# Kernel tuning notes

Measured on AMD Instinct MI355X. Metric: run time of the kernel, lower is better.

The kernel has to match this reference:

```python
import jax, jax.numpy as jnp
import numpy as np

B, S, C = 4, 4096, 128
C4 = C // 4  # q/k channels
OUT = 128    # == in_features, required by value @ weight


def setup_inputs() -> dict:
    key = jax.random.key(0)
    ks = jax.random.split(key, 9)
    stdv = 1.0 / np.sqrt(OUT)
    u = lambda k, shape, s: jax.random.uniform(k, shape, jnp.float32, -s, s)
    kaiming = lambda k, shape: u(k, shape, float(1.0 / np.sqrt(shape[1])))
    return {
        "x": jax.random.normal(ks[0], (B, S, C), jnp.float32),
        "weight": u(ks[1], (C, OUT), stdv),      # GCN weight [in, out]
        "bias": u(ks[2], (OUT,), stdv),
        "wq": kaiming(ks[3], (C4, C)),           # conv1d k=1 == linear [out_ch, in_ch]
        "bq": u(ks[4], (C4,), float(1.0 / np.sqrt(C))),
        "wk": kaiming(ks[5], (C4, C)),
        "bk": u(ks[6], (C4,), float(1.0 / np.sqrt(C))),
        "wv": kaiming(ks[7], (OUT, C)),
        "bv": u(ks[8], (OUT,), float(1.0 / np.sqrt(C))),
    }


def reference(x, weight, bias, wq, bq, wk, bk, wv, bv):
    # conv1d with kernel_size=1 == per-position linear projection
    q = jnp.einsum("bsc,qc->bsq", x, wq) + bq        # [B,S,C4] (query, pre-permute it is [B,C4,S])
    k = jnp.einsum("bsc,qc->bsq", x, wk) + bk        # [B,S,C4]
    # scores[i,j] = key_i . query_j  (unscaled), softmax over j
    scores = jnp.einsum("bic,bjc->bij", k, q)        # [B,S,S]
    adj = jax.nn.softmax(scores, axis=-1)
    v = jnp.einsum("bsc,oc->bso", x, wv) + bv        # [B,S,OUT]
    support = jnp.einsum("bso,ou->bsu", v, weight)   # [B,S,OUT]
    out = jnp.einsum("bij,bju->biu", adj, support)   # [B,S,OUT]
    return out + bias
```

## Files before the change

kernel.cpp:

```cpp
#include <hip/hip_runtime.h>

#define NB   4
#define SEQ  4096
#define CIN  128
#define C4D  32
#define OUTC 128
#define LOG2E 1.44269504f

typedef __attribute__((ext_vector_type(8))) short bf16x8;
typedef __attribute__((ext_vector_type(4))) float f32x4;

__device__ __forceinline__ short f2bf(float f) {
  union { float f; unsigned u; } v; v.f = f;
  unsigned r = v.u + 0x7FFFu + ((v.u >> 16) & 1u);
  return (short)(r >> 16);
}

__device__ __forceinline__ unsigned cvt_pk_bf16(float lo, float hi) {
  unsigned r;
  asm("v_cvt_pk_bf16_f32 %0, %1, %2" : "=v"(r) : "v"(lo), "v"(hi));
  return r;
}

__device__ __forceinline__ float fast_exp2(float x) {
  float r;
  asm("v_exp_f32 %0, %1" : "=v"(r) : "v"(x));
  return r;
}

__device__ __forceinline__ f32x4 mfma16(bf16x8 a, bf16x8 b, f32x4 c) {
  return __builtin_amdgcn_mfma_f32_16x16x32_bf16(a, b, c, 0, 0, 0);
}

__device__ __forceinline__ void gload_lds16(const short* g, short* l) {
  __builtin_amdgcn_global_load_lds(
      (const __attribute__((address_space(1))) void*)(g),
      (__attribute__((address_space(3))) void*)(l), 16, 0, 0);
}

__global__ void k_fuse(const float* __restrict__ wq, const float* __restrict__ wk,
                       const float* __restrict__ wv, const float* __restrict__ weight,
                       const float* __restrict__ bv,
                       short* __restrict__ wqb, short* __restrict__ wkb,
                       short* __restrict__ wfT, float* __restrict__ bfu) {
  int u = blockIdx.x, c = threadIdx.x;
  float acc = 0.f;
  for (int o = 0; o < OUTC; ++o) acc += wv[o * CIN + c] * weight[o * OUTC + u];
  wfT[u * CIN + c] = f2bf(acc);
  if (u < C4D) {
    wqb[u * CIN + c] = f2bf(wq[u * CIN + c]);
    wkb[u * CIN + c] = f2bf(wk[u * CIN + c]);
  }
  if (c == 0) {
    float a = 0.f;
    for (int o = 0; o < OUTC; ++o) a += bv[o] * weight[o * OUTC + u];
    bfu[u] = a;
  }
}

__global__ __launch_bounds__(256) void k_proj(
    const float* __restrict__ x, const float* __restrict__ bq, const float* __restrict__ bk,
    const short* __restrict__ wqb, const short* __restrict__ wkb,
    const short* __restrict__ wfT, const float* __restrict__ bfu,
    short* __restrict__ ql, short* __restrict__ kb, short* __restrict__ vfb) {
  const int wid = threadIdx.x >> 6, lane = threadIdx.x & 63;
  const int lo = lane & 15, g = lane >> 4;
  const int p0 = blockIdx.x * 64 + wid * 16;

  f32x4 aq[2] = {}, ak[2] = {}, as_[8] = {};

#pragma unroll
  for (int kk = 0; kk < 4; ++kk) {
    const float* xp = x + (size_t)(p0 + lo) * CIN + kk * 32 + g * 8;
    float4 xa = *(const float4*)xp;
    float4 xb = *(const float4*)(xp + 4);
    bf16x8 af;
    af[0] = f2bf(xa.x); af[1] = f2bf(xa.y); af[2] = f2bf(xa.z); af[3] = f2bf(xa.w);
    af[4] = f2bf(xb.x); af[5] = f2bf(xb.y); af[6] = f2bf(xb.z); af[7] = f2bf(xb.w);
#pragma unroll
    for (int n = 0; n < 2; ++n) {
      bf16x8 bq_ = *(const bf16x8*)(wqb + (size_t)(n * 16 + lo) * CIN + kk * 32 + g * 8);
      aq[n] = mfma16(af, bq_, aq[n]);
      bf16x8 bk_ = *(const bf16x8*)(wkb + (size_t)(n * 16 + lo) * CIN + kk * 32 + g * 8);
      ak[n] = mfma16(af, bk_, ak[n]);
    }
#pragma unroll
    for (int n = 0; n < 8; ++n) {
      bf16x8 bs = *(const bf16x8*)(wfT + (size_t)(n * 16 + lo) * CIN + kk * 32 + g * 8);
      as_[n] = mfma16(af, bs, as_[n]);
    }
  }

#pragma unroll
  for (int n = 0; n < 2; ++n) {
    float bqv = bq[n * 16 + lo], bkv = bk[n * 16 + lo];
    int u = n * 16 + lo;
#pragma unroll
    for (int r = 0; r < 4; ++r) {
      int p = p0 + 4 * g + r;
      int bb = p >> 12, s = p & (SEQ - 1);
      ql[(size_t)bb * (SEQ * 32) + (size_t)(s >> 5) * 1024 + ((s >> 4) & 1) * 512 +
         (u >> 3) * 128 + (s & 15) * 8 + (u & 7)] = f2bf(aq[n][r] + bqv);
      kb[(size_t)p * C4D + u] = f2bf((ak[n][r] + bkv) * LOG2E);
    }
  }
  {
    const int p = p0 + 4 * g;
    const int bb = p >> 12, s = p & (SEQ - 1);
#pragma unroll
    for (int n = 0; n < 8; ++n) {
      int u = n * 16 + lo;
      float bvv = bfu[u];
      uint2 w;
      w.x = cvt_pk_bf16(as_[n][0] + bvv, as_[n][1] + bvv);
      w.y = cvt_pk_bf16(as_[n][2] + bvv, as_[n][3] + bvv);
      *(uint2*)&vfb[(size_t)bb * (SEQ * 128) + (size_t)(s >> 5) * 4096 + (u >> 4) * 512 +
                    ((s >> 2) & 3) * 128 + (u & 15) * 8 + ((s >> 4) & 1) * 4] = w;
    }
  }
}

__global__ __launch_bounds__(512, 2) void k_attn(
    const short* __restrict__ ql, const short* __restrict__ kb,
    const short* __restrict__ vfb, const float* __restrict__ bias,
    float* __restrict__ out) {
  const int tid = threadIdx.x;
  const int wid = tid >> 6, lane = tid & 63;
  const int lo = lane & 15, g = lane >> 4;
  const int bid = blockIdx.x;
  const int xb = ((bid & 7) << 5) | (bid >> 3);
  const int b = xb >> 6;
  const int iw = (xb & 63) * 64;

  __shared__ __align__(16) char smem[133120];
  short* Vs = (short*)smem;
  float* LDSF = (float*)smem;

  const short* qB = ql + (size_t)b * (SEQ * 32) + (size_t)wid * 16384;
  const short* vB = vfb + (size_t)b * (SEQ * 128) + (size_t)wid * 65536;
  short* Vw = Vs + wid * 8192;

  bf16x8 kf[4];
#pragma unroll
  for (int c = 0; c < 4; ++c)
    kf[c] = *(const bf16x8*)(kb + (size_t)(b * SEQ + iw + 16 * c + lo) * C4D + g * 8);

  f32x4 o[4][8];
#pragma unroll
  for (int c = 0; c < 4; ++c)
#pragma unroll
    for (int n = 0; n < 8; ++n) o[c][n] = (f32x4){0.f, 0.f, 0.f, 0.f};

  float ma[4] = {-3e38f, -3e38f, -3e38f, -3e38f};
  float la[4] = {0.f, 0.f, 0.f, 0.f};
  const f32x4 zf = {0.f, 0.f, 0.f, 0.f};

  bf16x8 pf[4];

  bf16x8 qf0 = *(const bf16x8*)(qB + lane * 8);
  bf16x8 qf1 = *(const bf16x8*)(qB + 512 + lane * 8);
#pragma unroll
  for (int n = 0; n < 8; ++n)
    gload_lds16(vB + n * 512 + lane * 8, Vw + n * 512);

#pragma unroll 2
  for (int t = 0; t < 16; ++t) {
    const int cur = t & 1, nxt = cur ^ 1;

    f32x4 s0[4], s1[4];
    float tm[4];
#pragma unroll
    for (int c = 0; c < 4; ++c) {
      s0[c] = mfma16(qf0, kf[c], zf);
      s1[c] = mfma16(qf1, kf[c], zf);
      tm[c] = fmaxf(fmaxf(fmaxf(s0[c][0], s0[c][1]), fmaxf(s0[c][2], s0[c][3])),
                    fmaxf(fmaxf(s1[c][0], s1[c][1]), fmaxf(s1[c][2], s1[c][3])));
    }

    if (t + 1 < 16) {
      const short* qt = qB + (size_t)(t + 1) * 1024;
      qf0 = *(const bf16x8*)(qt + lane * 8);
      qf1 = *(const bf16x8*)(qt + 512 + lane * 8);
      const short* vn = vB + (size_t)(t + 1) * 4096;
      short* vd = Vw + nxt * 4096;
#pragma unroll
      for (int n = 0; n < 8; ++n)
        gload_lds16(vn + n * 512 + lane * 8, vd + n * 512);
    }

    bool need = (tm[0] > ma[0] + 11.5f) | (tm[1] > ma[1] + 11.5f) |
                (tm[2] > ma[2] + 11.5f) | (tm[3] > ma[3] + 11.5f);
    if (__any(need)) {
#pragma unroll
      for (int c = 0; c < 4; ++c) {
        float rowm = fmaxf(tm[c], __shfl_xor(tm[c], 16, 64));
        rowm = fmaxf(rowm, __shfl_xor(rowm, 32, 64));
        float mnew = fmaxf(ma[c], rowm);
        float scale = fast_exp2(ma[c] - mnew);
        la[c] *= scale;
        float sc[4];
#pragma unroll
        for (int r = 0; r < 4; ++r) sc[r] = __shfl(scale, 4 * g + r, 64);
#pragma unroll
        for (int n = 0; n < 8; ++n)
#pragma unroll
          for (int r = 0; r < 4; ++r) o[c][n][r] *= sc[r];
        ma[c] = mnew;
      }
    }

#pragma unroll
    for (int c = 0; c < 4; ++c) {
      float p[8];
#pragma unroll
      for (int r = 0; r < 4; ++r) {
        p[r]     = fast_exp2(s0[c][r] - ma[c]);
        p[4 + r] = fast_exp2(s1[c][r] - ma[c]);
      }
      la[c] += (p[0] + p[1]) + (p[2] + p[3]) + ((p[4] + p[5]) + (p[6] + p[7]));
      union { bf16x8 v8; unsigned u[4]; } pk;
      pk.u[0] = cvt_pk_bf16(p[0], p[1]);
      pk.u[1] = cvt_pk_bf16(p[2], p[3]);
      pk.u[2] = cvt_pk_bf16(p[4], p[5]);
      pk.u[3] = cvt_pk_bf16(p[6], p[7]);
      pf[c] = pk.v8;
    }

    asm volatile("s_waitcnt vmcnt(10)" ::: "memory");

    const short* vt = Vw + cur * 4096;
#pragma unroll
    for (int n = 0; n < 8; ++n) {
      bf16x8 vfr = *(const bf16x8*)(vt + n * 512 + lane * 8);
      o[0][n] = mfma16(pf[0], vfr, o[0][n]);
      o[1][n] = mfma16(pf[1], vfr, o[1][n]);
      o[2][n] = mfma16(pf[2], vfr, o[2][n]);
      o[3][n] = mfma16(pf[3], vfr, o[3][n]);
    }
  }

#pragma unroll
  for (int c = 0; c < 4; ++c) {
    la[c] += __shfl_xor(la[c], 16, 64);
    la[c] += __shfl_xor(la[c], 32, 64);
  }

  __syncthreads();

  auto write_slot = [&](int s) {
    float* OSs = LDSF + s * 8192;
#pragma unroll
    for (int c = 0; c < 4; ++c)
#pragma unroll
      for (int n = 0; n < 8; ++n)
        *(f32x4*)&OSs[(c * 8 + n) * 256 + lane * 4] = o[c][n];
    if (lane < 16) {
#pragma unroll
      for (int c = 0; c < 4; ++c) {
        LDSF[32768 + s * 64 + c * 16 + lo] = ma[c];
        LDSF[33024 + s * 64 + c * 16 + lo] = la[c];
      }
    }
  };
  auto merge_slot = [&](int s) {
    float* OSs = LDSF + s * 8192;
#pragma unroll
    for (int c = 0; c < 4; ++c) {
      float ms = LDSF[32768 + s * 64 + c * 16 + lo];
      float ls = LDSF[33024 + s * 64 + c * 16 + lo];
      float M = fmaxf(ma[c], ms);
      float eo = fast_exp2(ma[c] - M), es = fast_exp2(ms - M);
      la[c] = eo * la[c] + es * ls;
      ma[c] = M;
      float eor[4], esr[4];
#pragma unroll
      for (int r = 0; r < 4; ++r) {
        eor[r] = __shfl(eo, 4 * g + r, 64);
        esr[r] = __shfl(es, 4 * g + r, 64);
      }
#pragma unroll
      for (int n = 0; n < 8; ++n) {
        f32x4 v = *(f32x4*)&OSs[(c * 8 + n) * 256 + lane * 4];
#pragma unroll
        for (int r = 0; r < 4; ++r)
          o[c][n][r] = eor[r] * o[c][n][r] + esr[r] * v[r];
      }
    }
  };

  if (wid >= 4) write_slot(wid - 4);
  __syncthreads();
  if (wid < 4) merge_slot(wid);
  __syncthreads();
  if (wid == 1) write_slot(0);
  if (wid == 3) write_slot(1);
  __syncthreads();
  if (wid == 0) merge_slot(0);
  if (wid == 2) merge_slot(1);
  __syncthreads();
  if (wid == 2) write_slot(0);
  __syncthreads();
  if (wid == 0) {
    merge_slot(0);
    float* outp = out + (size_t)(b * SEQ + iw) * OUTC;
#pragma unroll
    for (int c = 0; c < 4; ++c) {
      float ia = 1.f / la[c];
      float lir[4];
#pragma unroll
      for (int r = 0; r < 4; ++r) lir[r] = __shfl(ia, 4 * g + r, 64);
#pragma unroll
      for (int n = 0; n < 8; ++n) {
        float bu = bias[n * 16 + lo];
#pragma unroll
        for (int r = 0; r < 4; ++r)
          outp[(size_t)(c * 16 + 4 * g + r) * OUTC + n * 16 + lo] =
              o[c][n][r] * lir[r] + bu;
      }
    }
  }
}

extern "C" void kernel_launch(void* const* d_in, const int* in_sizes, int n_in,
                              void* d_out, int out_size, void* d_ws, size_t ws_size,
                              hipStream_t stream) {
  (void)in_sizes; (void)n_in; (void)out_size; (void)ws_size;
  const float* x      = (const float*)d_in[0];
  const float* weight = (const float*)d_in[1];
  const float* bias   = (const float*)d_in[2];
  const float* wq     = (const float*)d_in[3];
  const float* bq     = (const float*)d_in[4];
  const float* wk     = (const float*)d_in[5];
  const float* bk     = (const float*)d_in[6];
  const float* wv     = (const float*)d_in[7];
  const float* bv     = (const float*)d_in[8];
  float* out = (float*)d_out;

  char* ws = (char*)d_ws;
  short* kbuf = (short*)(ws);
  short* vfb  = (short*)(ws + ((size_t)1 << 20));
  short* qlb  = (short*)(ws + ((size_t)5 << 20));
  short* wqb  = (short*)(ws + ((size_t)6 << 20));
  short* wkb  = (short*)(ws + ((size_t)6 << 20) + 8192);
  short* wfT  = (short*)(ws + ((size_t)6 << 20) + 16384);
  float* bfu  = (float*)(ws + ((size_t)6 << 20) + 49152);

  hipLaunchKernelGGL(k_fuse, dim3(OUTC), dim3(CIN), 0, stream,
                     wq, wk, wv, weight, bv, wqb, wkb, wfT, bfu);
  hipLaunchKernelGGL(k_proj, dim3(NB * SEQ / 64), dim3(256), 0, stream,
                     x, bq, bk, wqb, wkb, wfT, bfu, qlb, kbuf, vfb);
  hipLaunchKernelGGL(k_attn, dim3(NB * SEQ / 64), dim3(512), 0, stream,
                     qlb, kbuf, vfb, bias, out);
}
```

Baseline: 58.67 us.

## Stage projection weights in swizzled LDS, set MFMA priority, unroll fuse reductions

k_proj now copies the bf16 q/k/fused-value weights, which sit contiguously in the workspace, into a 48 KB LDS buffer with an XOR swizzle. MFMA operands are then read from LDS instead of global memory each iteration. The attention loop wraps its MFMA bursts in s_setprio so the wave gets issue priority during matrix work. k_fuse splits its reductions across several accumulators to break the serial add chains. The cost is extra LDS use per block, which may lower k_proj occupancy, plus a block-wide sync before compute.

```diff
diff --git a/kernel.cpp b/kernel.cpp
--- a/kernel.cpp
+++ b/kernel.cpp
@@ -44,28 +44,52 @@
                        short* __restrict__ wqb, short* __restrict__ wkb,
                        short* __restrict__ wfT, float* __restrict__ bfu) {
   int u = blockIdx.x, c = threadIdx.x;
-  float acc = 0.f;
-  for (int o = 0; o < OUTC; ++o) acc += wv[o * CIN + c] * weight[o * OUTC + u];
-  wfT[u * CIN + c] = f2bf(acc);
+  float a0 = 0.f, a1 = 0.f, a2 = 0.f, a3 = 0.f;
+  for (int o = 0; o < OUTC; o += 4) {
+    a0 += wv[(o + 0) * CIN + c] * weight[(o + 0) * OUTC + u];
+    a1 += wv[(o + 1) * CIN + c] * weight[(o + 1) * OUTC + u];
+    a2 += wv[(o + 2) * CIN + c] * weight[(o + 2) * OUTC + u];
+    a3 += wv[(o + 3) * CIN + c] * weight[(o + 3) * OUTC + u];
+  }
+  wfT[u * CIN + c] = f2bf((a0 + a1) + (a2 + a3));
   if (u < C4D) {
     wqb[u * CIN + c] = f2bf(wq[u * CIN + c]);
     wkb[u * CIN + c] = f2bf(wk[u * CIN + c]);
   }
   if (c == 0) {
-    float a = 0.f;
-    for (int o = 0; o < OUTC; ++o) a += bv[o] * weight[o * OUTC + u];
-    bfu[u] = a;
-  }
+    float b0 = 0.f, b1 = 0.f;
+    for (int o = 0; o < OUTC; o += 2) {
+      b0 += bv[o] * weight[o * OUTC + u];
+      b1 += bv[o + 1] * weight[(o + 1) * OUTC + u];
+    }
+    bfu[u] = b0 + b1;
+  }
+}
+
+__device__ __forceinline__ int wswz(int byte) {
+  return byte ^ (((byte >> 8) & 7) << 4);
 }
 
 __global__ __launch_bounds__(256) void k_proj(
     const float* __restrict__ x, const float* __restrict__ bq, const float* __restrict__ bk,
-    const short* __restrict__ wqb, const short* __restrict__ wkb,
-    const short* __restrict__ wfT, const float* __restrict__ bfu,
+    const short* __restrict__ wall, const float* __restrict__ bfu,
     short* __restrict__ ql, short* __restrict__ kb, short* __restrict__ vfb) {
-  const int wid = threadIdx.x >> 6, lane = threadIdx.x & 63;
+  const int tid = threadIdx.x;
+  const int wid = tid >> 6, lane = tid & 63;
   const int lo = lane & 15, g = lane >> 4;
   const int p0 = blockIdx.x * 64 + wid * 16;
+
+  __shared__ __align__(16) short WL[24576];
+#pragma unroll
+  for (int i = 0; i < 12; ++i) {
+    bf16x8 v = *(const bf16x8*)(wall + i * 2048 + tid * 8);
+    *(bf16x8*)((char*)WL + wswz((i * 2048 + tid * 8) * 2)) = v;
+  }
+  __syncthreads();
+
+  auto wfrag = [&](int idx) -> bf16x8 {
+    return *(const bf16x8*)((char*)WL + wswz(idx * 2));
+  };
 
   f32x4 aq[2] = {}, ak[2] = {}, as_[8] = {};
 
@@ -79,14 +103,14 @@
     af[4] = f2bf(xb.x); af[5] = f2bf(xb.y); af[6] = f2bf(xb.z); af[7] = f2bf(xb.w);
 #pragma unroll
     for (int n = 0; n < 2; ++n) {
-      bf16x8 bq_ = *(const bf16x8*)(wqb + (size_t)(n * 16 + lo) * CIN + kk * 32 + g * 8);
+      bf16x8 bq_ = wfrag((n * 16 + lo) * CIN + kk * 32 + g * 8);
       aq[n] = mfma16(af, bq_, aq[n]);
-      bf16x8 bk_ = *(const bf16x8*)(wkb + (size_t)(n * 16 + lo) * CIN + kk * 32 + g * 8);
+      bf16x8 bk_ = wfrag(4096 + (n * 16 + lo) * CIN + kk * 32 + g * 8);
       ak[n] = mfma16(af, bk_, ak[n]);
     }
 #pragma unroll
     for (int n = 0; n < 8; ++n) {
-      bf16x8 bs = *(const bf16x8*)(wfT + (size_t)(n * 16 + lo) * CIN + kk * 32 + g * 8);
+      bf16x8 bs = wfrag(8192 + (n * 16 + lo) * CIN + kk * 32 + g * 8);
       as_[n] = mfma16(af, bs, as_[n]);
     }
   }
@@ -169,10 +193,15 @@
 
     f32x4 s0[4], s1[4];
     float tm[4];
+    __builtin_amdgcn_s_setprio(1);
 #pragma unroll
     for (int c = 0; c < 4; ++c) {
       s0[c] = mfma16(qf0, kf[c], zf);
       s1[c] = mfma16(qf1, kf[c], zf);
+    }
+    __builtin_amdgcn_s_setprio(0);
+#pragma unroll
+    for (int c = 0; c < 4; ++c) {
       tm[c] = fmaxf(fmaxf(fmaxf(s0[c][0], s0[c][1]), fmaxf(s0[c][2], s0[c][3])),
                     fmaxf(fmaxf(s1[c][0], s1[c][1]), fmaxf(s1[c][2], s1[c][3])));
     }
@@ -229,6 +258,7 @@
     asm volatile("s_waitcnt vmcnt(10)" ::: "memory");
 
     const short* vt = Vw + cur * 4096;
+    __builtin_amdgcn_s_setprio(1);
 #pragma unroll
     for (int n = 0; n < 8; ++n) {
       bf16x8 vfr = *(const bf16x8*)(vt + n * 512 + lane * 8);
@@ -237,6 +267,7 @@
       o[2][n] = mfma16(pf[2], vfr, o[2][n]);
       o[3][n] = mfma16(pf[3], vfr, o[3][n]);
     }
+    __builtin_amdgcn_s_setprio(0);
   }
 
 #pragma unroll
@@ -348,7 +379,7 @@
   hipLaunchKernelGGL(k_fuse, dim3(OUTC), dim3(CIN), 0, stream,
                      wq, wk, wv, weight, bv, wqb, wkb, wfT, bfu);
   hipLaunchKernelGGL(k_proj, dim3(NB * SEQ / 64), dim3(256), 0, stream,
-                     x, bq, bk, wqb, wkb, wfT, bfu, qlb, kbuf, vfb);
+                     x, bq, bk, wqb , bfu, qlb, kbuf, vfb);
   hipLaunchKernelGGL(k_attn, dim3(NB * SEQ / 64), dim3(512), 0, stream,
                      qlb, kbuf, vfb, bias, out);
 }
```

Result: faster. 53.06 us (-9.6%).
